# Kernel optimization log

Measured on AMD Instinct MI355X. Metric: run time of the kernel, lower is better.

Reference implementation:

```python
import jax, jax.numpy as jnp
import numpy as np

B, L, D = 4, 4096, 768
ORDER = 2
EMB = 33      # HyenaFilter emb_dim default
FFN = 64      # filter_order
FREQ = 10.0


def setup_inputs() -> dict:
    key = jax.random.key(0)
    ks = jax.random.split(key, 10)
    def rn(i, shape, scale):
        return jax.random.normal(ks[i], shape, dtype=jnp.float32) * scale
    return {
        "u": jax.random.normal(ks[0], (B, L, D), dtype=jnp.float32),
        "W_in": rn(1, (D, (ORDER + 1) * D), 0.02),
        "b_in": jnp.zeros(((ORDER + 1) * D,), jnp.float32),
        "conv_k": rn(2, (3, (ORDER + 1) * D), 0.3),   # depthwise kernel, 3 taps
        "conv_b": jnp.zeros(((ORDER + 1) * D,), jnp.float32),
        "W1": rn(3, (EMB, FFN), 0.1),
        "b1": jnp.zeros((FFN,), jnp.float32),
        "W2": rn(4, (FFN, ORDER * D), 0.05),
        "b2": jnp.zeros((ORDER * D,), jnp.float32),
        "f_bias": rn(5, (ORDER, D), 0.05),
        "f_decay": rn(6, (ORDER, D), 0.05),
        "W_out": rn(7, (D, D), 0.02),
        "b_out": jnp.zeros((D,), jnp.float32),
    }


def _hyena_filter(W1, b1, W2, b2, f_bias, f_decay):
    # Implicit filter: sinusoidal positional features -> MLP with sin activation
    t = jnp.linspace(0.0, 1.0, L)[:, None]                      # [L,1]
    bands = jnp.linspace(0.0, float(EMB - 1), EMB)[None, :]     # [1,EMB]
    pe = jnp.sin(t * bands * FREQ)                              # [L,EMB]
    h = jnp.sin(FREQ * (pe @ W1 + b1))                          # [L,FFN]
    h = h @ W2 + b2                                             # [L,ORDER*D]
    h = h.reshape(L, ORDER, D).transpose(1, 2, 0)               # [ORDER,D,L]
    t_window = jnp.linspace(0.0, float(L), L)[None, None, :]    # [1,1,L]
    decay = jnp.exp(-jnp.exp(f_decay)[:, :, None] * t_window)   # [ORDER,D,L]
    return h * decay + f_bias[:, :, None]


def reference(u, W_in, b_in, conv_k, conv_b, W1, b1, W2, b2,
              f_bias, f_decay, W_out, b_out):
    # input projection: [B,L,D] -> [B,L,(ORDER+1)*D]
    proj = u @ W_in + b_in
    # depthwise causal conv, kernel_size=3 (pad 2 on the left)
    xp = jnp.pad(proj, ((0, 0), (2, 0), (0, 0)))
    proj = (xp[:, 0:L, :] * conv_k[0]
            + xp[:, 1:L + 1, :] * conv_k[1]
            + xp[:, 2:L + 2, :] * conv_k[2]) + conv_b
    proj = proj.reshape(B, L, ORDER + 1, D).transpose(0, 2, 3, 1)  # [B,ORDER+1,D,L]
    x = proj[:, :ORDER]   # gates, [B,ORDER,D,L]
    v = proj[:, ORDER]    # value, [B,D,L]

    h = _hyena_filter(W1, b1, W2, b2, f_bias, f_decay)  # [ORDER,D,L]

    n_fft = 2 * L  # zero-padded linear convolution via rfft
    for n in range(ORDER):
        v_f = jnp.fft.rfft(v, n=n_fft, axis=-1)          # [B,D,L+1] complex
        h_f = jnp.fft.rfft(h[n], n=n_fft, axis=-1)       # [D,L+1] complex
        y = jnp.fft.irfft(v_f * h_f[None], n=n_fft, axis=-1)[..., :L]
        v = y * x[:, n]                                   # gated recurrence

    return v.transpose(0, 2, 1) @ W_out + b_out           # [B,L,D]
```

## Files before the change

### kernel.cpp

```cpp
#include <hip/hip_runtime.h>
#include <math.h>

#define L_SEQ 4096
#define D_DIM 768
#define C3    2304
#define TAPS  32

typedef __attribute__((ext_vector_type(8))) short bf16x8;
typedef __attribute__((ext_vector_type(4))) float f32x4;

__device__ __forceinline__ unsigned short f2bf(float x) {
  union { float f; unsigned u; } v; v.f = x;
  unsigned r = v.u + 0x7FFF + ((v.u >> 16) & 1);
  return (unsigned short)(r >> 16);
}
__device__ __forceinline__ float bf2f(unsigned short u) {
  union { unsigned u; float f; } v; v.u = ((unsigned)u) << 16; return v.f;
}
__device__ __forceinline__ void gld_lds16(const void* g, void* l) {
  __builtin_amdgcn_global_load_lds((const __attribute__((address_space(1))) void*)g,
                                   (__attribute__((address_space(3))) void*)l, 16, 0, 0);
}

__global__ __launch_bounds__(256) void filt_kernel(const float* __restrict__ W1,
                                                   const float* __restrict__ b1,
                                                   const float* __restrict__ W2,
                                                   const float* __restrict__ b2,
                                                   const float* __restrict__ f_decay,
                                                   float* __restrict__ g_tab) {
  __shared__ float phi_s[2048];
  const int tid = threadIdx.x;
  #pragma unroll
  for (int it = 0; it < 8; ++it) {
    int idx = tid + it * 256;
    int t = idx >> 6, f = idx & 63;
    float tt = (float)t / 4095.0f;
    float s = b1[f];
    #pragma unroll
    for (int e = 0; e < 33; ++e)
      s += sinf(tt * (float)e * 10.0f) * W1[e * 64 + f];
    phi_s[idx] = sinf(10.0f * s);
  }
  __syncthreads();
  int idx = blockIdx.x * 256 + tid;
  int c2 = idx >> 5, t = idx & 31;
  float acc = b2[c2];
  #pragma unroll 8
  for (int f = 0; f < 64; ++f)
    acc += phi_s[t * 64 + f] * W2[f * 1536 + c2];
  float r = expf(f_decay[c2]);
  g_tab[idx] = acc * expf(-r * (float)t * (4096.0f / 4095.0f));
}

__global__ __launch_bounds__(256) void cvt_kernel(const float* __restrict__ src,
                                                  unsigned short* __restrict__ dst) {
  int idx = (blockIdx.x * 256 + threadIdx.x) * 4;
  float4 v = *(const float4*)&src[idx];
  ushort4 o;
  o.x = f2bf(v.x); o.y = f2bf(v.y); o.z = f2bf(v.z); o.w = f2bf(v.w);
  *(ushort4*)&dst[idx] = o;
}

__global__ __launch_bounds__(256) void wtrans_kernel(const float* __restrict__ W_in,
                                                     unsigned short* __restrict__ W_inT,
                                                     const float* __restrict__ W_out,
                                                     unsigned short* __restrict__ W_outT) {
  __shared__ float t[32][33];
  const int z = blockIdx.z;
  const float* src = z ? W_out : W_in;
  unsigned short* dst = z ? W_outT : W_inT;
  const int C = z ? 768 : 2304;
  const int c0 = blockIdx.x * 32, r0 = blockIdx.y * 32;
  if (c0 >= C) return;
  const int tx = threadIdx.x & 31, ty = threadIdx.x >> 5;
  #pragma unroll
  for (int rr = 0; rr < 4; ++rr)
    t[ty + rr * 8][tx] = src[(long)(r0 + ty + rr * 8) * C + c0 + tx];
  __syncthreads();
  #pragma unroll
  for (int rr = 0; rr < 4; ++rr)
    dst[(long)(c0 + ty + rr * 8) * 768 + r0 + tx] = f2bf(t[tx][ty + rr * 8]);
}

#define G1_BUF 16384
__global__ __launch_bounds__(256) void gemm1_mfma(const unsigned short* __restrict__ A,
                                                  const unsigned short* __restrict__ Bt,
                                                  const float* __restrict__ bias,
                                                  unsigned short* __restrict__ proj) {
  __shared__ __align__(16) char smem[32768];
  const int tid = threadIdx.x;
  const int w = tid >> 6, lane = tid & 63;
  const int lr = tid >> 2, lc = tid & 3;
  const int id = blockIdx.y * 18 + blockIdx.x;
  const int x8 = id & 7, j = id >> 3;
  const int m0 = (x8 * 16 + j / 18) * 128;
  const int n0 = (j % 18) * 128;
  const int wm = (w & 1) * 64, wn = (w >> 1) * 64;
  const int fm = lane & 15, fk = lane >> 4;
  f32x4 acc[4][4] = {};
  const unsigned short* Ag = A + (size_t)(m0 + lr) * 768 + lc * 8;
  const unsigned short* Bg = Bt + (size_t)(n0 + lr) * 768 + lc * 8;

  {
    char* dst = smem + tid * 16;
    gld_lds16(Ag,            dst);
    gld_lds16(Ag + 64 * 768, dst + 4096);
    gld_lds16(Bg,            dst + 8192);
    gld_lds16(Bg + 64 * 768, dst + 12288);
  }
  for (int kk = 0; kk < 24; ++kk) {
    const int cur = (kk & 1) * G1_BUF;
    __syncthreads();
    if (kk < 23) {
      const int k0 = (kk + 1) * 32;
      char* dst = smem + ((kk + 1) & 1) * G1_BUF + tid * 16;
      gld_lds16(Ag + k0,            dst);
      gld_lds16(Ag + k0 + 64 * 768, dst + 4096);
      gld_lds16(Bg + k0,            dst + 8192);
      gld_lds16(Bg + k0 + 64 * 768, dst + 12288);
    }
    const unsigned short* As = (const unsigned short*)(smem + cur);
    const unsigned short* Bs = As + 4096;
    bf16x8 af[4], bfr[4];
    #pragma unroll
    for (int i = 0; i < 4; ++i) af[i]  = *(const bf16x8*)&As[(wm + i * 16 + fm) * 32 + fk * 8];
    #pragma unroll
    for (int j2 = 0; j2 < 4; ++j2) bfr[j2] = *(const bf16x8*)&Bs[(wn + j2 * 16 + fm) * 32 + fk * 8];
    #pragma unroll
    for (int i = 0; i < 4; ++i)
      #pragma unroll
      for (int j2 = 0; j2 < 4; ++j2)
        acc[i][j2] = __builtin_amdgcn_mfma_f32_16x16x32_bf16(af[i], bfr[j2], acc[i][j2], 0, 0, 0);
  }

  const int b = m0 >> 12, l0 = m0 & 4095;
  float* fbuf = (float*)smem;
  #pragma unroll
  for (int cg = 0; cg < 4; ++cg) {
    __syncthreads();
    #pragma unroll
    for (int i = 0; i < 4; ++i)
      *(f32x4*)&fbuf[w * 1088 + fm * 68 + i * 16 + fk * 4] = acc[i][cg];
    __syncthreads();
    #pragma unroll
    for (int p = 0; p < 4; ++p) {
      int nl = p * 4 + fk;
      int c = n0 + wn + cg * 16 + nl;
      float4 v = *(float4*)&fbuf[w * 1088 + nl * 68 + fm * 4];
      float bb = bias[c];
      ushort4 o;
      o.x = f2bf(v.x + bb); o.y = f2bf(v.y + bb); o.z = f2bf(v.z + bb); o.w = f2bf(v.w + bb);
      *(ushort4*)&proj[((size_t)b * C3 + c) * L_SEQ + l0 + wm + fm * 4] = o;
    }
  }
}

#define G2_BUF 12288
__global__ __launch_bounds__(256) void gemm2_mfma(const unsigned short* __restrict__ A,
                                                  const unsigned short* __restrict__ Bt,
                                                  const float* __restrict__ bias,
                                                  float* __restrict__ out) {
  __shared__ __align__(16) char smem[24576];
  const int tid = threadIdx.x;
  const int w = tid >> 6, lane = tid & 63;
  const int lr = tid >> 2, lc = tid & 3;
  const int id = blockIdx.y * 6 + blockIdx.x;
  const int x8 = id & 7, j = id >> 3;
  const int m0 = (x8 * 32 + j / 6) * 64;
  const int n0 = (j % 6) * 128;
  const int wm = (w & 1) * 32, wn = (w >> 1) * 64;
  const int fm = lane & 15, fk = lane >> 4;
  f32x4 acc[2][4] = {};
  const unsigned short* Ag = A + (size_t)(m0 + lr) * 768 + lc * 8;
  const unsigned short* Bg = Bt + (size_t)(n0 + lr) * 768 + lc * 8;

  {
    char* dst = smem + tid * 16;
    gld_lds16(Ag,            dst);
    gld_lds16(Bg,            dst + 4096);
    gld_lds16(Bg + 64 * 768, dst + 8192);
  }
  for (int kk = 0; kk < 24; ++kk) {
    const int cur = (kk & 1) * G2_BUF;
    __syncthreads();
    if (kk < 23) {
      const int k0 = (kk + 1) * 32;
      char* dst = smem + ((kk + 1) & 1) * G2_BUF + tid * 16;
      gld_lds16(Ag + k0,            dst);
      gld_lds16(Bg + k0,            dst + 4096);
      gld_lds16(Bg + k0 + 64 * 768, dst + 8192);
    }
    const unsigned short* As = (const unsigned short*)(smem + cur);
    const unsigned short* Bs = As + 2048;
    bf16x8 af[2], bfr[4];
    #pragma unroll
    for (int i = 0; i < 2; ++i) af[i]  = *(const bf16x8*)&As[(wm + i * 16 + fm) * 32 + fk * 8];
    #pragma unroll
    for (int j2 = 0; j2 < 4; ++j2) bfr[j2] = *(const bf16x8*)&Bs[(wn + j2 * 16 + fm) * 32 + fk * 8];
    #pragma unroll
    for (int i = 0; i < 2; ++i)
      #pragma unroll
      for (int j2 = 0; j2 < 4; ++j2)
        acc[i][j2] = __builtin_amdgcn_mfma_f32_16x16x32_bf16(af[i], bfr[j2], acc[i][j2], 0, 0, 0);
  }

  float* fbuf = (float*)smem + w * 1088;
  const int nf = lane & 15, mq = lane >> 4;
  float4 bb4 = *(const float4*)&bias[n0 + wn + nf * 4];
  #pragma unroll
  for (int i = 0; i < 2; ++i) {
    __syncthreads();
    #pragma unroll
    for (int cg = 0; cg < 4; ++cg)
      #pragma unroll
      for (int r = 0; r < 4; ++r)
        fbuf[(fk * 4 + r) * 68 + cg * 16 + fm] = acc[i][cg][r];
    __syncthreads();
    #pragma unroll
    for (int pass = 0; pass < 4; ++pass) {
      int m_l = pass * 4 + mq;
      float4 v = *(float4*)&fbuf[m_l * 68 + nf * 4];
      v.x += bb4.x; v.y += bb4.y; v.z += bb4.z; v.w += bb4.w;
      *(float4*)&out[(size_t)(m0 + wm + i * 16 + m_l) * D_DIM + n0 + wn + nf * 4] = v;
    }
  }
}

__global__ __launch_bounds__(256) void row_kernel(const unsigned short* __restrict__ proj,
                                                  unsigned short* __restrict__ v2T,
                                                  const float* __restrict__ conv_k,
                                                  const float* __restrict__ conv_b,
                                                  const float* __restrict__ g_tab,
                                                  const float* __restrict__ f_bias) {
  __shared__ float buf0[4128];
  __shared__ float buf1[4128];
  __shared__ float sgs[2 * TAPS];
  __shared__ float wsum[4];
  __shared__ float bnd[3][4][2];
  const int tid = threadIdx.x;
  const int lane = tid & 63, w = tid >> 6;
  const int b = blockIdx.x / D_DIM, d = blockIdx.x % D_DIM;
  const int g = tid * 16;

  const unsigned short* rowV  = proj + ((size_t)b * C3 + 2 * D_DIM + d) * L_SEQ;
  const unsigned short* rowX0 = proj + ((size_t)b * C3 + d) * L_SEQ;
  const unsigned short* rowX1 = proj + ((size_t)b * C3 + D_DIM + d) * L_SEQ;

  float v[16], x0[16], x1[16];
  #pragma unroll
  for (int k = 0; k < 4; ++k) {
    ushort4 qv = *(const ushort4*)&rowV[g + k * 4];
    v[k * 4] = bf2f(qv.x); v[k * 4 + 1] = bf2f(qv.y); v[k * 4 + 2] = bf2f(qv.z); v[k * 4 + 3] = bf2f(qv.w);
    ushort4 q0 = *(const ushort4*)&rowX0[g + k * 4];
    x0[k * 4] = bf2f(q0.x); x0[k * 4 + 1] = bf2f(q0.y); x0[k * 4 + 2] = bf2f(q0.z); x0[k * 4 + 3] = bf2f(q0.w);
    ushort4 q1 = *(const ushort4*)&rowX1[g + k * 4];
    x1[k * 4] = bf2f(q1.x); x1[k * 4 + 1] = bf2f(q1.y); x1[k * 4 + 2] = bf2f(q1.z); x1[k * 4 + 3] = bf2f(q1.w);
  }

  if (tid < 32) {
    int ph = (tid & 15) * 258 + (tid >> 4);
    buf0[ph] = 0.f; buf1[ph] = 0.f;
  }
  if (tid < 64) sgs[tid] = g_tab[((size_t)((tid >> 5) * D_DIM + d)) * TAPS + (tid & 31)];
  if (lane == 63) {
    bnd[0][w][0] = v[14];  bnd[0][w][1] = v[15];
    bnd[1][w][0] = x0[14]; bnd[1][w][1] = x0[15];
    bnd[2][w][0] = x1[14]; bnd[2][w][1] = x1[15];
  }
  const int cv = 2 * D_DIM + d, cx0 = d, cx1 = D_DIM + d;
  const float kv0 = conv_k[cv],  kv1 = conv_k[C3 + cv],  kv2 = conv_k[2 * C3 + cv],  bv = conv_b[cv];
  const float ka0 = conv_k[cx0], ka1 = conv_k[C3 + cx0], ka2 = conv_k[2 * C3 + cx0], ba = conv_b[cx0];
  const float kb0 = conv_k[cx1], kb1 = conv_k[C3 + cx1], kb2 = conv_k[2 * C3 + cx1], bb = conv_b[cx1];
  const float fb0 = f_bias[d], fb1 = f_bias[D_DIM + d];
  __syncthreads();

  float vm1 = __shfl_up(v[15], 1),  vm2 = __shfl_up(v[14], 1);
  float am1 = __shfl_up(x0[15], 1), am2 = __shfl_up(x0[14], 1);
  float bm1 = __shfl_up(x1[15], 1), bm2 = __shfl_up(x1[14], 1);
  if (lane == 0) {
    if (w > 0) {
      vm2 = bnd[0][w-1][0]; vm1 = bnd[0][w-1][1];
      am2 = bnd[1][w-1][0]; am1 = bnd[1][w-1][1];
      bm2 = bnd[2][w-1][0]; bm1 = bnd[2][w-1][1];
    } else {
      vm1 = vm2 = am1 = am2 = bm1 = bm2 = 0.f;
    }
  }
  float r[16];
  r[0] = vm2 * kv0 + vm1 * kv1 + v[0] * kv2 + bv;
  r[1] = vm1 * kv0 + v[0] * kv1 + v[1] * kv2 + bv;
  #pragma unroll
  for (int i = 2; i < 16; ++i) r[i] = v[i-2] * kv0 + v[i-1] * kv1 + v[i] * kv2 + bv;
  {
    float t0 = am2 * ka0 + am1 * ka1 + x0[0] * ka2 + ba;
    float t1 = am1 * ka0 + x0[0] * ka1 + x0[1] * ka2 + ba;
    #pragma unroll
    for (int i = 15; i >= 2; --i) x0[i] = x0[i-2] * ka0 + x0[i-1] * ka1 + x0[i] * ka2 + ba;
    x0[0] = t0; x0[1] = t1;
  }
  {
    float t0 = bm2 * kb0 + bm1 * kb1 + x1[0] * kb2 + bb;
    float t1 = bm1 * kb0 + x1[0] * kb1 + x1[1] * kb2 + bb;
    #pragma unroll
    for (int i = 15; i >= 2; --i) x1[i] = x1[i-2] * kb0 + x1[i-1] * kb1 + x1[i] * kb2 + bb;
    x1[0] = t0; x1[1] = t1;
  }
  #pragma unroll
  for (int i = 0; i < 16; ++i) buf0[i * 258 + tid + 2] = r[i];
  __syncthreads();

  float h[32];
  #pragma unroll
  for (int j = 0; j < 32; ++j) h[j] = buf0[(j & 15) * 258 + tid + (j >> 4)];
  float p[16], run = 0.f;
  #pragma unroll
  for (int i = 0; i < 16; ++i) { run += r[i]; p[i] = run; }
  float s = run;
  #pragma unroll
  for (int off = 1; off < 64; off <<= 1) {
    float o = __shfl_up(s, off);
    if (lane >= off) s += o;
  }
  if (lane == 63) wsum[w] = s;
  __syncthreads();
  float woff = 0.f;
  #pragma unroll
  for (int k = 0; k < 4; ++k) if (k < w) woff += wsum[k];
  float excl = woff + s - run;
  float y0[16];
  #pragma unroll
  for (int i = 0; i < 16; ++i) {
    float a = fb0 * (excl + p[i]);
    #pragma unroll
    for (int t = 0; t < TAPS; ++t) {
      float vv = (t <= i) ? r[i - t] : h[32 + i - t];
      a += sgs[t] * vv;
    }
    y0[i] = a * x0[i];
  }
  #pragma unroll
  for (int i = 0; i < 16; ++i) buf1[i * 258 + tid + 2] = y0[i];
  __syncthreads();

  #pragma unroll
  for (int j = 0; j < 32; ++j) h[j] = buf1[(j & 15) * 258 + tid + (j >> 4)];
  run = 0.f;
  #pragma unroll
  for (int i = 0; i < 16; ++i) { run += y0[i]; p[i] = run; }
  s = run;
  #pragma unroll
  for (int off = 1; off < 64; off <<= 1) {
    float o = __shfl_up(s, off);
    if (lane >= off) s += o;
  }
  if (lane == 63) wsum[w] = s;
  __syncthreads();
  woff = 0.f;
  #pragma unroll
  for (int k = 0; k < 4; ++k) if (k < w) woff += wsum[k];
  excl = woff + s - run;
  unsigned short yout[16];
  #pragma unroll
  for (int i = 0; i < 16; ++i) {
    float a = fb1 * (excl + p[i]);
    #pragma unroll
    for (int t = 0; t < TAPS; ++t) {
      float vv = (t <= i) ? y0[i - t] : h[32 + i - t];
      a += sgs[TAPS + t] * vv;
    }
    yout[i] = f2bf(a * x1[i]);
  }
  unsigned short* outRow = v2T + ((size_t)b * D_DIM + d) * L_SEQ + g;
  *(ushort4*)&outRow[0]  = *(ushort4*)&yout[0];
  *(ushort4*)&outRow[4]  = *(ushort4*)&yout[4];
  *(ushort4*)&outRow[8]  = *(ushort4*)&yout[8];
  *(ushort4*)&outRow[12] = *(ushort4*)&yout[12];
}

__global__ __launch_bounds__(256) void transpose_v2(const unsigned short* __restrict__ src,
                                                    unsigned short* __restrict__ dst) {
  __shared__ unsigned short t[64][66];
  const int l0 = blockIdx.x * 64, d0 = blockIdx.y * 64, b = blockIdx.z;
  const int tx = threadIdx.x & 31, ty = threadIdx.x >> 5;
  const unsigned short* s = src + ((size_t)b * D_DIM + d0) * L_SEQ + l0;
  #pragma unroll
  for (int r = 0; r < 8; ++r) {
    int dd = ty + r * 8;
    *(ushort2*)&t[dd][tx * 2] = *(const ushort2*)&s[(size_t)dd * L_SEQ + tx * 2];
  }
  __syncthreads();
  unsigned short* q = dst + ((size_t)b * L_SEQ + l0) * D_DIM + d0;
  #pragma unroll
  for (int r = 0; r < 8; ++r) {
    int ll = ty + r * 8;
    ushort2 v; v.x = t[tx * 2][ll]; v.y = t[tx * 2 + 1][ll];
    *(ushort2*)&q[(size_t)ll * D_DIM + tx * 2] = v;
  }
}

extern "C" void kernel_launch(void* const* d_in, const int* in_sizes, int n_in,
                              void* d_out, int out_size, void* d_ws, size_t ws_size,
                              hipStream_t stream) {
  (void)in_sizes; (void)n_in; (void)out_size; (void)ws_size;
  const float* u       = (const float*)d_in[0];
  const float* W_in    = (const float*)d_in[1];
  const float* b_in    = (const float*)d_in[2];
  const float* conv_k  = (const float*)d_in[3];
  const float* conv_b  = (const float*)d_in[4];
  const float* W1      = (const float*)d_in[5];
  const float* b1      = (const float*)d_in[6];
  const float* W2      = (const float*)d_in[7];
  const float* b2      = (const float*)d_in[8];
  const float* f_bias  = (const float*)d_in[9];
  const float* f_decay = (const float*)d_in[10];
  const float* W_out   = (const float*)d_in[11];
  const float* b_out   = (const float*)d_in[12];
  float* out = (float*)d_out;

  unsigned short* proj  = (unsigned short*)d_ws;
  unsigned short* v2T   = proj + (size_t)4 * C3 * L_SEQ;
  unsigned short* ubf   = v2T + (size_t)4 * D_DIM * L_SEQ;
  unsigned short* v2F   = ubf;
  unsigned short* W_inT = ubf + (size_t)16384 * 768;
  unsigned short* W_outT= W_inT + (size_t)C3 * D_DIM;
  float* g_tab          = (float*)(W_outT + (size_t)D_DIM * D_DIM);

  filt_kernel<<<192, 256, 0, stream>>>(W1, b1, W2, b2, f_decay, g_tab);
  cvt_kernel<<<12288, 256, 0, stream>>>(u, ubf);
  wtrans_kernel<<<dim3(72, 24, 2), 256, 0, stream>>>(W_in, W_inT, W_out, W_outT);
  gemm1_mfma<<<dim3(18, 128), 256, 0, stream>>>(ubf, W_inT, b_in, proj);
  row_kernel<<<3072, 256, 0, stream>>>(proj, v2T, conv_k, conv_b, g_tab, f_bias);
  transpose_v2<<<dim3(64, 12, 4), 256, 0, stream>>>(v2T, v2F);
  gemm2_mfma<<<dim3(6, 256), 256, 0, stream>>>(v2F, W_outT, b_out, out);
}
```

Baseline: 308.2 us.

## Rewrite input-projection GEMM as 256x256-tile, 4-stage pipelined 8-wave kernel

Replaces the 128x128 double-buffered input-projection GEMM with a 256x256 tile kernel of 512 threads that uses a 4-stage LDS ring (128KB of dynamic shared memory). Global-to-LDS loads are issued several k-steps ahead and throttled with explicit vmcnt waits. MFMA phases are separated by s_barrier and set to higher priority with setprio. The epilogue writes accumulators straight to global memory instead of staging them through LDS. The aim is more data reuse per tile and better overlap of loads with MFMA work, at the cost of heavy LDS use, limited occupancy, and hand-tuned synchronization that is fragile.

```diff
diff --git a/kernel.cpp b/kernel.cpp
--- a/kernel.cpp
+++ b/kernel.cpp
@@ -82,75 +82,121 @@
     dst[(long)(c0 + ty + rr * 8) * 768 + r0 + tx] = f2bf(t[tx][ty + rr * 8]);
 }
 
-#define G1_BUF 16384
-__global__ __launch_bounds__(256) void gemm1_mfma(const unsigned short* __restrict__ A,
-                                                  const unsigned short* __restrict__ Bt,
-                                                  const float* __restrict__ bias,
-                                                  unsigned short* __restrict__ proj) {
-  __shared__ __align__(16) char smem[32768];
+__device__ __forceinline__ void g1_vmwait(int VM) {
+  if (VM == 8)      asm volatile("s_waitcnt vmcnt(8)" ::: "memory");
+  else if (VM == 4) asm volatile("s_waitcnt vmcnt(4)" ::: "memory");
+  else if (VM == 0) asm volatile("s_waitcnt vmcnt(0)" ::: "memory");
+}
+
+template<bool STG, int VM>
+__device__ __forceinline__ void g1_step(int kt, char* smemc, int tid,
+                                        int wm128, int wn64, int fm, int fk8,
+                                        const unsigned short* aP, const unsigned short* bP,
+                                        f32x4 (&acc)[8][4]) {
+  const int s = kt & 3;
+  const unsigned short* As = (const unsigned short*)(smemc + s * 32768);
+  const unsigned short* Bs = (const unsigned short*)(smemc + s * 32768 + 16384);
+  bf16x8 af[4], bfr[4];
+  #pragma unroll
+  for (int i = 0; i < 4; ++i) af[i]  = *(const bf16x8*)&As[(wm128 + i * 16 + fm) * 32 + fk8];
+  #pragma unroll
+  for (int jj = 0; jj < 4; ++jj) bfr[jj] = *(const bf16x8*)&Bs[(wn64 + jj * 16 + fm) * 32 + fk8];
+  if (STG) {
+    const unsigned short* ap = aP + (kt + 3) * 32;
+    char* d = smemc + ((kt + 3) & 3) * 32768 + tid * 16;
+    gld_lds16(ap,         d);
+    gld_lds16(ap + 98304, d + 8192);
+  }
+  asm volatile("" ::: "memory");
+  __builtin_amdgcn_s_barrier();
+  __builtin_amdgcn_s_setprio(1);
+  __builtin_amdgcn_sched_barrier(0);
+  #pragma unroll
+  for (int i = 0; i < 4; ++i)
+    #pragma unroll
+    for (int jj = 0; jj < 4; ++jj)
+      acc[i][jj] = __builtin_amdgcn_mfma_f32_16x16x32_bf16(af[i], bfr[jj], acc[i][jj], 0, 0, 0);
+  __builtin_amdgcn_sched_barrier(0);
+  __builtin_amdgcn_s_setprio(0);
+  asm volatile("" ::: "memory");
+  __builtin_amdgcn_s_barrier();
+  bf16x8 ag[4];
+  #pragma unroll
+  for (int i = 0; i < 4; ++i) ag[i] = *(const bf16x8*)&As[(wm128 + (i + 4) * 16 + fm) * 32 + fk8];
+  if (STG) {
+    const unsigned short* bp = bP + (kt + 3) * 32;
+    char* d = smemc + ((kt + 3) & 3) * 32768 + 16384 + tid * 16;
+    gld_lds16(bp,         d);
+    gld_lds16(bp + 98304, d + 8192);
+  }
+  asm volatile("" ::: "memory");
+  __builtin_amdgcn_s_barrier();
+  __builtin_amdgcn_s_setprio(1);
+  __builtin_amdgcn_sched_barrier(0);
+  #pragma unroll
+  for (int i = 0; i < 4; ++i)
+    #pragma unroll
+    for (int jj = 0; jj < 4; ++jj)
+      acc[i + 4][jj] = __builtin_amdgcn_mfma_f32_16x16x32_bf16(ag[i], bfr[jj], acc[i + 4][jj], 0, 0, 0);
+  __builtin_amdgcn_sched_barrier(0);
+  __builtin_amdgcn_s_setprio(0);
+  g1_vmwait(VM);
+  asm volatile("" ::: "memory");
+  __builtin_amdgcn_s_barrier();
+}
+
+__global__ __launch_bounds__(512, 2) void gemm1_8ph(const unsigned short* __restrict__ A,
+                                                    const unsigned short* __restrict__ Bt,
+                                                    const float* __restrict__ bias,
+                                                    unsigned short* __restrict__ proj) {
+  extern __shared__ char smemc[];
   const int tid = threadIdx.x;
   const int w = tid >> 6, lane = tid & 63;
-  const int lr = tid >> 2, lc = tid & 3;
-  const int id = blockIdx.y * 18 + blockIdx.x;
-  const int x8 = id & 7, j = id >> 3;
-  const int m0 = (x8 * 16 + j / 18) * 128;
-  const int n0 = (j % 18) * 128;
-  const int wm = (w & 1) * 64, wn = (w >> 1) * 64;
-  const int fm = lane & 15, fk = lane >> 4;
-  f32x4 acc[4][4] = {};
-  const unsigned short* Ag = A + (size_t)(m0 + lr) * 768 + lc * 8;
-  const unsigned short* Bg = Bt + (size_t)(n0 + lr) * 768 + lc * 8;
-
-  {
-    char* dst = smem + tid * 16;
-    gld_lds16(Ag,            dst);
-    gld_lds16(Ag + 64 * 768, dst + 4096);
-    gld_lds16(Bg,            dst + 8192);
-    gld_lds16(Bg + 64 * 768, dst + 12288);
-  }
-  for (int kk = 0; kk < 24; ++kk) {
-    const int cur = (kk & 1) * G1_BUF;
-    __syncthreads();
-    if (kk < 23) {
-      const int k0 = (kk + 1) * 32;
-      char* dst = smem + ((kk + 1) & 1) * G1_BUF + tid * 16;
-      gld_lds16(Ag + k0,            dst);
-      gld_lds16(Ag + k0 + 64 * 768, dst + 4096);
-      gld_lds16(Bg + k0,            dst + 8192);
-      gld_lds16(Bg + k0 + 64 * 768, dst + 12288);
-    }
-    const unsigned short* As = (const unsigned short*)(smem + cur);
-    const unsigned short* Bs = As + 4096;
-    bf16x8 af[4], bfr[4];
-    #pragma unroll
-    for (int i = 0; i < 4; ++i) af[i]  = *(const bf16x8*)&As[(wm + i * 16 + fm) * 32 + fk * 8];
-    #pragma unroll
-    for (int j2 = 0; j2 < 4; ++j2) bfr[j2] = *(const bf16x8*)&Bs[(wn + j2 * 16 + fm) * 32 + fk * 8];
-    #pragma unroll
-    for (int i = 0; i < 4; ++i)
-      #pragma unroll
-      for (int j2 = 0; j2 < 4; ++j2)
-        acc[i][j2] = __builtin_amdgcn_mfma_f32_16x16x32_bf16(af[i], bfr[j2], acc[i][j2], 0, 0, 0);
-  }
+  const int id = blockIdx.x;
+  const int x8 = id & 7, jb = id >> 3;
+  const int mt = x8 * 8 + jb / 9, nt = jb % 9;
+  const int m0 = mt * 256, n0 = nt * 256;
+  const int wm128 = (w >> 2) * 128, wn64 = (w & 3) * 64;
+  const int fm = lane & 15, fk8 = (lane >> 4) * 8;
+  const unsigned short* aP = A  + (size_t)(m0 + (tid >> 2)) * 768 + (tid & 3) * 8;
+  const unsigned short* bP = Bt + (size_t)(n0 + (tid >> 2)) * 768 + (tid & 3) * 8;
+  f32x4 acc[8][4] = {};
+
+  #pragma unroll
+  for (int kt = 0; kt < 3; ++kt) {
+    char* d = smemc + kt * 32768 + tid * 16;
+    const unsigned short* ap = aP + kt * 32;
+    const unsigned short* bp = bP + kt * 32;
+    gld_lds16(ap,         d);
+    gld_lds16(ap + 98304, d + 8192);
+    gld_lds16(bp,         d + 16384);
+    gld_lds16(bp + 98304, d + 24576);
+  }
+  asm volatile("s_waitcnt vmcnt(8)" ::: "memory");
+  asm volatile("" ::: "memory");
+  __builtin_amdgcn_s_barrier();
+
+  #pragma unroll 1
+  for (int kt = 0; kt < 21; ++kt)
+    g1_step<true, 8>(kt, smemc, tid, wm128, wn64, fm, fk8, aP, bP, acc);
+  g1_step<false, 4>(21, smemc, tid, wm128, wn64, fm, fk8, aP, bP, acc);
+  g1_step<false, 0>(22, smemc, tid, wm128, wn64, fm, fk8, aP, bP, acc);
+  g1_step<false, -1>(23, smemc, tid, wm128, wn64, fm, fk8, aP, bP, acc);
 
   const int b = m0 >> 12, l0 = m0 & 4095;
-  float* fbuf = (float*)smem;
-  #pragma unroll
-  for (int cg = 0; cg < 4; ++cg) {
-    __syncthreads();
-    #pragma unroll
-    for (int i = 0; i < 4; ++i)
-      *(f32x4*)&fbuf[w * 1088 + fm * 68 + i * 16 + fk * 4] = acc[i][cg];
-    __syncthreads();
-    #pragma unroll
-    for (int p = 0; p < 4; ++p) {
-      int nl = p * 4 + fk;
-      int c = n0 + wn + cg * 16 + nl;
-      float4 v = *(float4*)&fbuf[w * 1088 + nl * 68 + fm * 4];
-      float bb = bias[c];
+  const int fk4 = (fk8 >> 3) * 4;
+  #pragma unroll
+  for (int j2 = 0; j2 < 4; ++j2) {
+    int c = n0 + wn64 + j2 * 16 + fm;
+    float bb = bias[c];
+    unsigned short* pr = proj + ((size_t)b * C3 + c) * L_SEQ + l0 + wm128 + fk4;
+    #pragma unroll
+    for (int i = 0; i < 8; ++i) {
+      f32x4 a = acc[i][j2];
       ushort4 o;
-      o.x = f2bf(v.x + bb); o.y = f2bf(v.y + bb); o.z = f2bf(v.z + bb); o.w = f2bf(v.w + bb);
-      *(ushort4*)&proj[((size_t)b * C3 + c) * L_SEQ + l0 + wm + fm * 4] = o;
+      o.x = f2bf(a[0] + bb); o.y = f2bf(a[1] + bb);
+      o.z = f2bf(a[2] + bb); o.w = f2bf(a[3] + bb);
+      *(ushort4*)&pr[i * 16] = o;
     }
   }
 }
@@ -425,10 +471,17 @@
   unsigned short* W_outT= W_inT + (size_t)C3 * D_DIM;
   float* g_tab          = (float*)(W_outT + (size_t)D_DIM * D_DIM);
 
+  static bool g1_attr = false;
+  if (!g1_attr) {
+    (void)hipFuncSetAttribute(reinterpret_cast<const void*>(gemm1_8ph),
+                              hipFuncAttributeMaxDynamicSharedMemorySize, 131072);
+    g1_attr = true;
+  }
+
   filt_kernel<<<192, 256, 0, stream>>>(W1, b1, W2, b2, f_decay, g_tab);
   cvt_kernel<<<12288, 256, 0, stream>>>(u, ubf);
   wtrans_kernel<<<dim3(72, 24, 2), 256, 0, stream>>>(W_in, W_inT, W_out, W_outT);
-  gemm1_mfma<<<dim3(18, 128), 256, 0, stream>>>(ubf, W_inT, b_in, proj);
+  gemm1_8ph<<<576, 512, 131072, stream>>>(ubf, W_inT, b_in, proj);
   row_kernel<<<3072, 256, 0, stream>>>(proj, v2T, conv_k, conv_b, g_tab, f_bias);
   transpose_v2<<<dim3(64, 12, 4), 256, 0, stream>>>(v2T, v2F);
   gemm2_mfma<<<dim3(6, 256), 256, 0, stream>>>(v2F, W_outT, b_out, out);
```

Result: slower. 325.8 us (+5.7%).
